# Kernel tuning notes

Hardware: AMD Instinct MI355X
Metric: run time of the kernel (lower is better)

## Reference

```python
import jax, jax.numpy as jnp
import numpy as np


def setup_inputs() -> dict:
    key = jax.random.key(0)
    k1, k2 = jax.random.split(key)
    B, C, N = 32, 512, 4096
    x = jax.random.normal(k1, (B, C, N), dtype=jnp.float32)
    gamma = jax.random.normal(k2, (1,), dtype=jnp.float32)
    return {"x": x, "gamma": gamma}


def reference(x, gamma):
    # x: [B, C, N]. Channel attention: energy = x @ x^T -> [B, C, C]
    energy = jnp.einsum('bcn,bdn->bcd', x, x)
    # inverted score: rowmax - energy, then softmax over last dim
    energy_new = jnp.max(energy, axis=-1, keepdims=True) - energy
    attention = jax.nn.softmax(energy_new, axis=-1)  # [B, C, C]
    out = jnp.einsum('bcd,bdn->bcn', attention, x)
    return gamma * out + x
```

## Files before the change

kernel.cpp:

```cpp
#include <hip/hip_runtime.h>
#include <stdint.h>
#include <stddef.h>

#define NB 32
#define NC 512
#define NN 4096
#define NSPLIT 4
#define KCH (NN / NSPLIT)

typedef _Float16 h4_t __attribute__((ext_vector_type(4)));
typedef _Float16 h8_t __attribute__((ext_vector_type(8)));
typedef float    f4_t __attribute__((ext_vector_type(4)));

__device__ __forceinline__ void gload16(const _Float16* g, _Float16* l) {
    __builtin_amdgcn_global_load_lds(
        (const __attribute__((address_space(1))) void*)g,
        (__attribute__((address_space(3))) void*)l, 16, 0, 0);
}

__global__ __launch_bounds__(256) void cast_transpose(
    const float* __restrict__ x, _Float16* __restrict__ Xh,
    _Float16* __restrict__ Xl, _Float16* __restrict__ Xt)
{
    __shared__ __attribute__((aligned(16))) _Float16 tile[64 * 66];
    const int b = blockIdx.z, c0 = blockIdx.y * 64, n0 = blockIdx.x * 64;
    const int t = threadIdx.x;
    const int lr = t >> 4;
    const int lc = (t & 15) * 4;
    const size_t xbase = (size_t)b * NC * NN;

#pragma unroll
    for (int p = 0; p < 4; ++p) {
        const int r = p * 16 + lr;
        const size_t off = xbase + (size_t)(c0 + r) * NN + (n0 + lc);
        const float4 v = *(const float4*)(x + off);
        const _Float16 h0 = (_Float16)v.x, h1 = (_Float16)v.y;
        const _Float16 h2 = (_Float16)v.z, h3 = (_Float16)v.w;
        h4_t hv = {h0, h1, h2, h3};
        *(h4_t*)(Xh + off) = hv;
        h4_t lv = {(_Float16)(v.x - (float)h0), (_Float16)(v.y - (float)h1),
                   (_Float16)(v.z - (float)h2), (_Float16)(v.w - (float)h3)};
        *(h4_t*)(Xl + off) = lv;
        tile[r * 66 + lc + 0] = h0;
        tile[r * 66 + lc + 1] = h1;
        tile[r * 66 + lc + 2] = h2;
        tile[r * 66 + lc + 3] = h3;
    }
    __syncthreads();
    const size_t tbase = (size_t)b * NN * NC;
#pragma unroll
    for (int p = 0; p < 4; ++p) {
        const int rn = p * 16 + lr;
        h4_t w;
        w[0] = tile[(lc + 0) * 66 + rn];
        w[1] = tile[(lc + 1) * 66 + rn];
        w[2] = tile[(lc + 2) * 66 + rn];
        w[3] = tile[(lc + 3) * 66 + rn];
        *(h4_t*)(Xt + tbase + (size_t)(n0 + rn) * NC + (c0 + lc)) = w;
    }
}

__global__ __launch_bounds__(256) void cast_hl(
    const float* __restrict__ x, _Float16* __restrict__ Xh,
    _Float16* __restrict__ Xl)
{
    const size_t total = (size_t)NB * NC * NN / 4;
    for (size_t i = (size_t)blockIdx.x * 256 + threadIdx.x; i < total;
         i += (size_t)gridDim.x * 256) {
        const float4 v = ((const float4*)x)[i];
        const _Float16 h0 = (_Float16)v.x, h1 = (_Float16)v.y;
        const _Float16 h2 = (_Float16)v.z, h3 = (_Float16)v.w;
        h4_t hv = {h0, h1, h2, h3};
        h4_t lv = {(_Float16)(v.x - (float)h0), (_Float16)(v.y - (float)h1),
                   (_Float16)(v.z - (float)h2), (_Float16)(v.w - (float)h3)};
        ((h4_t*)Xh)[i] = hv;
        ((h4_t*)Xl)[i] = lv;
    }
}

__global__ __launch_bounds__(256, 4) void gemm1_energy(
    const _Float16* __restrict__ Xh, const _Float16* __restrict__ Xl,
    float* __restrict__ part)
{
    __shared__ __attribute__((aligned(16))) _Float16 sAh[128 * 32];
    __shared__ __attribute__((aligned(16))) _Float16 sBh[128 * 32];
    __shared__ __attribute__((aligned(16))) _Float16 sAl[128 * 32];
    __shared__ __attribute__((aligned(16))) _Float16 sBl[128 * 32];

    const int flat = blockIdx.x;
    const int xcd  = flat & 7;
    const int slot = flat >> 3;
    const int grp  = xcd + 8 * (slot / 10);
    const int mem  = slot % 10;
    const int b    = grp >> 2;
    const int s    = grp & (NSPLIT - 1);

    const int ti = (int)((sqrtf(8.0f * (float)mem + 1.0f) - 1.0f) * 0.5f);
    const int tj = mem - ((ti * (ti + 1)) >> 1);
    const bool diag = (ti == tj);

    const int t = threadIdx.x;
    const int wave = t >> 6, lane = t & 63;
    const int srow = t >> 2, scol = (t & 3) * 8;

    const size_t xb = (size_t)b * NC * NN + (size_t)s * KCH;
    const _Float16* gAh = Xh + xb + (size_t)(ti * 128 + srow) * NN + scol;
    const _Float16* gBh = Xh + xb + (size_t)(tj * 128 + srow) * NN + scol;
    const _Float16* gAl = Xl + xb + (size_t)(ti * 128 + srow) * NN + scol;
    const _Float16* gBl = Xl + xb + (size_t)(tj * 128 + srow) * NN + scol;

    const int wr = wave >> 1, wc = wave & 1;
    const int fr = lane & 15, fko = (lane >> 4) * 8;
    const int hi4 = (lane >> 4) * 4;

    const _Float16* rBh = diag ? sAh : sBh;
    const _Float16* rBl = diag ? sAl : sBl;

    f4_t acc[4][4];
#pragma unroll
    for (int m = 0; m < 4; ++m)
#pragma unroll
        for (int n = 0; n < 4; ++n) acc[m][n] = (f4_t){0.f, 0.f, 0.f, 0.f};

    for (int k0 = 0; k0 < KCH; k0 += 32) {
        gload16(gAh + k0,                   sAh + wave * 512);
        gload16(gAh + k0 + 64 * (size_t)NN, sAh + 2048 + wave * 512);
        gload16(gAl + k0,                   sAl + wave * 512);
        gload16(gAl + k0 + 64 * (size_t)NN, sAl + 2048 + wave * 512);
        if (!diag) {
            gload16(gBh + k0,                   sBh + wave * 512);
            gload16(gBh + k0 + 64 * (size_t)NN, sBh + 2048 + wave * 512);
            gload16(gBl + k0,                   sBl + wave * 512);
            gload16(gBl + k0 + 64 * (size_t)NN, sBl + 2048 + wave * 512);
        }
        __syncthreads();

        h8_t ah[4], bh[4], al[4], bl[4];
#pragma unroll
        for (int m = 0; m < 4; ++m) {
            ah[m] = *(const h8_t*)(sAh + (wr * 64 + m * 16 + fr) * 32 + fko);
            bh[m] = *(const h8_t*)(rBh + (wc * 64 + m * 16 + fr) * 32 + fko);
            al[m] = *(const h8_t*)(sAl + (wr * 64 + m * 16 + fr) * 32 + fko);
            bl[m] = *(const h8_t*)(rBl + (wc * 64 + m * 16 + fr) * 32 + fko);
        }
#pragma unroll
        for (int m = 0; m < 4; ++m)
#pragma unroll
            for (int nf = 0; nf < 4; ++nf) {
                acc[nf][m] = __builtin_amdgcn_mfma_f32_16x16x32_f16(bh[nf], ah[m], acc[nf][m], 0, 0, 0);
                acc[nf][m] = __builtin_amdgcn_mfma_f32_16x16x32_f16(bl[nf], ah[m], acc[nf][m], 0, 0, 0);
                acc[nf][m] = __builtin_amdgcn_mfma_f32_16x16x32_f16(bh[nf], al[m], acc[nf][m], 0, 0, 0);
            }
        __syncthreads();
    }

    float* pb = part + ((size_t)s * NB + b) * (NC * NC);
#pragma unroll
    for (int m = 0; m < 4; ++m) {
        const int i = ti * 128 + wr * 64 + m * 16 + fr;
#pragma unroll
        for (int nf = 0; nf < 4; ++nf) {
            const int jjb = tj * 128 + wc * 64 + nf * 16 + hi4;
            *(f4_t*)(pb + (size_t)i * NC + jjb) = acc[nf][m];
            if (!diag) {
#pragma unroll
                for (int j = 0; j < 4; ++j)
                    pb[(size_t)(jjb + j) * NC + i] = acc[nf][m][j];
            }
        }
    }
}

__global__ __launch_bounds__(256) void softmax_inv(
    const float* __restrict__ part, _Float16* __restrict__ attn)
{
    const int row = blockIdx.x * 4 + (threadIdx.x >> 6);
    const int lane = threadIdx.x & 63;
    const size_t roff = (size_t)row * NC;

    float4 a0 = {0.f, 0.f, 0.f, 0.f}, a1 = {0.f, 0.f, 0.f, 0.f};
#pragma unroll
    for (int s = 0; s < NSPLIT; ++s) {
        const float4* p = (const float4*)(part + (size_t)s * NB * NC * NC + roff);
        const float4 v0 = p[lane], v1 = p[64 + lane];
        a0.x += v0.x; a0.y += v0.y; a0.z += v0.z; a0.w += v0.w;
        a1.x += v1.x; a1.y += v1.y; a1.z += v1.z; a1.w += v1.w;
    }

    float mn = fminf(fminf(fminf(a0.x, a0.y), fminf(a0.z, a0.w)),
                     fminf(fminf(a1.x, a1.y), fminf(a1.z, a1.w)));
#pragma unroll
    for (int off = 32; off; off >>= 1) mn = fminf(mn, __shfl_xor(mn, off));

    const float w0 = __expf(mn - a0.x), w1 = __expf(mn - a0.y);
    const float w2 = __expf(mn - a0.z), w3 = __expf(mn - a0.w);
    const float w4 = __expf(mn - a1.x), w5 = __expf(mn - a1.y);
    const float w6 = __expf(mn - a1.z), w7 = __expf(mn - a1.w);
    float sum = ((w0 + w1) + (w2 + w3)) + ((w4 + w5) + (w6 + w7));
#pragma unroll
    for (int off = 32; off; off >>= 1) sum += __shfl_xor(sum, off);
    const float inv = 1.0f / sum;

    h4_t o0 = {(_Float16)(w0 * inv), (_Float16)(w1 * inv),
               (_Float16)(w2 * inv), (_Float16)(w3 * inv)};
    h4_t o1 = {(_Float16)(w4 * inv), (_Float16)(w5 * inv),
               (_Float16)(w6 * inv), (_Float16)(w7 * inv)};
    ((h4_t*)(attn + roff))[lane] = o0;
    ((h4_t*)(attn + roff))[64 + lane] = o1;
}

__global__ __launch_bounds__(256) void transpose_h(
    const _Float16* __restrict__ Xh, _Float16* __restrict__ Xt)
{
    __shared__ __attribute__((aligned(16))) _Float16 tile[64 * 66];
    const int b = blockIdx.z, c0 = blockIdx.y * 64, n0 = blockIdx.x * 64;
    const int t = threadIdx.x;
    const int lr = t >> 4;
    const int lc = (t & 15) * 4;
    const size_t hbase = (size_t)b * NC * NN;

#pragma unroll
    for (int p = 0; p < 4; ++p) {
        const int r = p * 16 + lr;
        const h4_t v = *(const h4_t*)(Xh + hbase + (size_t)(c0 + r) * NN + (n0 + lc));
        tile[r * 66 + lc + 0] = v[0];
        tile[r * 66 + lc + 1] = v[1];
        tile[r * 66 + lc + 2] = v[2];
        tile[r * 66 + lc + 3] = v[3];
    }
    __syncthreads();
    const size_t tbase = (size_t)b * NN * NC;
#pragma unroll
    for (int p = 0; p < 4; ++p) {
        const int rn = p * 16 + lr;
        h4_t w;
        w[0] = tile[(lc + 0) * 66 + rn];
        w[1] = tile[(lc + 1) * 66 + rn];
        w[2] = tile[(lc + 2) * 66 + rn];
        w[3] = tile[(lc + 3) * 66 + rn];
        *(h4_t*)(Xt + tbase + (size_t)(n0 + rn) * NC + (c0 + lc)) = w;
    }
}

__global__ __launch_bounds__(256) void gemm2_out(
    const _Float16* __restrict__ attn, const _Float16* __restrict__ Xt,
    const _Float16* __restrict__ Xh, const float* __restrict__ gammap,
    float* __restrict__ out)
{
    __shared__ __attribute__((aligned(16))) _Float16 sA[128 * 32];
    __shared__ __attribute__((aligned(16))) _Float16 sB[128 * 32];

    const int flat = blockIdx.x;
    const int xcd  = flat & 7;
    const int slot = flat >> 3;
    const int b    = xcd + 8 * (slot >> 7);
    const int memb = slot & 127;
    const int brow = (memb & 3) * 128;
    const int bcol = (memb >> 2) * 128;

    const int t = threadIdx.x;
    const int wave = t >> 6, lane = t & 63;
    const int srow = t >> 2, scol = (t & 3) * 8;

    const _Float16* gA = attn + (size_t)b * NC * NC + (size_t)(brow + srow) * NC + scol;
    const _Float16* gB = Xt   + (size_t)b * NN * NC + (size_t)(bcol + srow) * NC + scol;

    const int wr = wave >> 1, wc = wave & 1;
    const int fr = lane & 15, fko = (lane >> 4) * 8;
    const int hi4 = (lane >> 4) * 4;

    f4_t acc[4][4];
#pragma unroll
    for (int m = 0; m < 4; ++m)
#pragma unroll
        for (int n = 0; n < 4; ++n) acc[m][n] = (f4_t){0.f, 0.f, 0.f, 0.f};

    for (int k0 = 0; k0 < NC; k0 += 32) {
        gload16(gA + k0,           sA + wave * 512);
        gload16(gA + k0 + 64 * NC, sA + 2048 + wave * 512);
        gload16(gB + k0,           sB + wave * 512);
        gload16(gB + k0 + 64 * NC, sB + 2048 + wave * 512);
        __syncthreads();

        h8_t a[4], bb[4];
#pragma unroll
        for (int m = 0; m < 4; ++m) {
            a[m]  = *(const h8_t*)(sA + (wr * 64 + m * 16 + fr) * 32 + fko);
            bb[m] = *(const h8_t*)(sB + (wc * 64 + m * 16 + fr) * 32 + fko);
        }
#pragma unroll
        for (int m = 0; m < 4; ++m)
#pragma unroll
            for (int nf = 0; nf < 4; ++nf)
                acc[nf][m] = __builtin_amdgcn_mfma_f32_16x16x32_f16(bb[nf], a[m], acc[nf][m], 0, 0, 0);
        __syncthreads();
    }

    const float g = gammap[0];
    const _Float16* xb = Xh + (size_t)b * NC * NN;
    float* ob = out + (size_t)b * NC * NN;
#pragma unroll
    for (int m = 0; m < 4; ++m) {
        const int c_ = brow + wr * 64 + m * 16 + fr;
#pragma unroll
        for (int nf = 0; nf < 4; ++nf) {
            const int n_ = bcol + wc * 64 + nf * 16 + hi4;
            const size_t off = (size_t)c_ * NN + n_;
            const h4_t xv = *(const h4_t*)(xb + off);
            f4_t o;
#pragma unroll
            for (int j = 0; j < 4; ++j)
                o[j] = g * acc[nf][m][j] + (float)xv[j];
            *(f4_t*)(ob + off) = o;
        }
    }
}

extern "C" void kernel_launch(void* const* d_in, const int* in_sizes, int n_in,
                              void* d_out, int out_size, void* d_ws, size_t ws_size,
                              hipStream_t stream)
{
    const float* x     = (const float*)d_in[0];
    const float* gamma = (const float*)d_in[1];
    float* out = (float*)d_out;
    char* ws = (char*)d_ws;

    if (ws_size >= 553648128ull) {
        _Float16* Xh   = (_Float16*)(ws);
        _Float16* Xl   = (_Float16*)(ws + 134217728ull);
        _Float16* Xt   = (_Float16*)(ws + 268435456ull);
        _Float16* attn = (_Float16*)(ws + 402653184ull);
        float*    part = (float*)   (ws + 419430400ull);

        cast_transpose<<<dim3(NN / 64, NC / 64, NB), 256, 0, stream>>>(x, Xh, Xl, Xt);
        gemm1_energy<<<dim3(10 * NSPLIT * NB), 256, 0, stream>>>(Xh, Xl, part);
        softmax_inv<<<dim3(NB * NC / 4), 256, 0, stream>>>(part, attn);
        gemm2_out<<<dim3(4096), 256, 0, stream>>>(attn, Xt, Xh, gamma, out);
    } else {
        _Float16* Xh   = (_Float16*)(ws);
        _Float16* XlXt = (_Float16*)(ws + 134217728ull);
        _Float16* attn = (_Float16*)(ws + 268435456ull);
        float*    part = (float*)   (ws + 285212672ull);

        cast_hl<<<dim3(2048), 256, 0, stream>>>(x, Xh, XlXt);
        gemm1_energy<<<dim3(10 * NSPLIT * NB), 256, 0, stream>>>(Xh, XlXt, part);
        softmax_inv<<<dim3(NB * NC / 4), 256, 0, stream>>>(part, attn);
        transpose_h<<<dim3(NN / 64, NC / 64, NB), 256, 0, stream>>>(Xh, XlXt);
        gemm2_out<<<dim3(4096), 256, 0, stream>>>(attn, XlXt, Xh, gamma, out);
    }
}
```

Baseline: 476.6 us.

## Swizzle LDS tiles and double-buffer gemm2 with A read from global

In the first GEMM, the global-to-LDS copy and the fragment reads now use an XOR swizzle on the column chunk, so the 16-byte LDS reads no longer hit the same banks. The output GEMM is restructured. The Xt tile now uses a double-buffered, swizzled LDS layout with 64-wide K steps, and the next tile is prefetched while the current one is computed. The attention (A) fragments now come straight from global memory instead of being staged through LDS. This removes LDS bank conflicts and half the barriers, and overlaps loads with MFMA work. The cost is redundant global reads of A across waves and more LDS per block.

```diff
diff --git a/kernel.cpp b/kernel.cpp
--- a/kernel.cpp
+++ b/kernel.cpp
@@ -101,7 +101,8 @@
 
     const int t = threadIdx.x;
     const int wave = t >> 6, lane = t & 63;
-    const int srow = t >> 2, scol = (t & 3) * 8;
+    const int srow = t >> 2;
+    const int scol = (((t & 3) ^ ((t >> 2) & 3)) * 8);
 
     const size_t xb = (size_t)b * NC * NN + (size_t)s * KCH;
     const _Float16* gAh = Xh + xb + (size_t)(ti * 128 + srow) * NN + scol;
@@ -112,6 +113,7 @@
     const int wr = wave >> 1, wc = wave & 1;
     const int fr = lane & 15, fko = (lane >> 4) * 8;
     const int hi4 = (lane >> 4) * 4;
+    const int fsw = fko ^ ((fr & 3) << 3);
 
     const _Float16* rBh = diag ? sAh : sBh;
     const _Float16* rBl = diag ? sAl : sBl;
@@ -138,10 +140,10 @@
         h8_t ah[4], bh[4], al[4], bl[4];
 #pragma unroll
         for (int m = 0; m < 4; ++m) {
-            ah[m] = *(const h8_t*)(sAh + (wr * 64 + m * 16 + fr) * 32 + fko);
-            bh[m] = *(const h8_t*)(rBh + (wc * 64 + m * 16 + fr) * 32 + fko);
-            al[m] = *(const h8_t*)(sAl + (wr * 64 + m * 16 + fr) * 32 + fko);
-            bl[m] = *(const h8_t*)(rBl + (wc * 64 + m * 16 + fr) * 32 + fko);
+            ah[m] = *(const h8_t*)(sAh + (wr * 64 + m * 16 + fr) * 32 + fsw);
+            bh[m] = *(const h8_t*)(rBh + (wc * 64 + m * 16 + fr) * 32 + fsw);
+            al[m] = *(const h8_t*)(sAl + (wr * 64 + m * 16 + fr) * 32 + fsw);
+            bl[m] = *(const h8_t*)(rBl + (wc * 64 + m * 16 + fr) * 32 + fsw);
         }
 #pragma unroll
         for (int m = 0; m < 4; ++m)
@@ -247,8 +249,7 @@
     const _Float16* __restrict__ Xh, const float* __restrict__ gammap,
     float* __restrict__ out)
 {
-    __shared__ __attribute__((aligned(16))) _Float16 sA[128 * 32];
-    __shared__ __attribute__((aligned(16))) _Float16 sB[128 * 32];
+    __shared__ __attribute__((aligned(16))) _Float16 sB[2][128 * 64];
 
     const int flat = blockIdx.x;
     const int xcd  = flat & 7;
@@ -260,14 +261,15 @@
 
     const int t = threadIdx.x;
     const int wave = t >> 6, lane = t & 63;
-    const int srow = t >> 2, scol = (t & 3) * 8;
-
-    const _Float16* gA = attn + (size_t)b * NC * NC + (size_t)(brow + srow) * NC + scol;
-    const _Float16* gB = Xt   + (size_t)b * NN * NC + (size_t)(bcol + srow) * NC + scol;
-
     const int wr = wave >> 1, wc = wave & 1;
     const int fr = lane & 15, fko = (lane >> 4) * 8;
     const int hi4 = (lane >> 4) * 4;
+    const int bsw = (fr & 7) << 3;
+
+    const int rr = t >> 3;
+    const int sck = (((t & 7) ^ (rr & 7)) * 8);
+    const _Float16* gB = Xt + (size_t)b * NN * NC + (size_t)bcol * NC;
+    const _Float16* gA = attn + (size_t)b * NC * NC;
 
     f4_t acc[4][4];
 #pragma unroll
@@ -275,26 +277,50 @@
 #pragma unroll
         for (int n = 0; n < 4; ++n) acc[m][n] = (f4_t){0.f, 0.f, 0.f, 0.f};
 
-    for (int k0 = 0; k0 < NC; k0 += 32) {
-        gload16(gA + k0,           sA + wave * 512);
-        gload16(gA + k0 + 64 * NC, sA + 2048 + wave * 512);
-        gload16(gB + k0,           sB + wave * 512);
-        gload16(gB + k0 + 64 * NC, sB + 2048 + wave * 512);
+#define STAGE_B(buf, k0)                                                     \
+    {                                                                        \
+        _Pragma("unroll")                                                    \
+        for (int p = 0; p < 4; ++p)                                          \
+            gload16(gB + (size_t)(p * 32 + rr) * NC + (k0) + sck,            \
+                    &sB[buf][0] + p * 2048 + wave * 512 + (lane)*8);         \
+    }
+
+    STAGE_B(0, 0);
+    __syncthreads();
+
+    int cur = 0;
+#pragma unroll
+    for (int it = 0; it < 8; ++it) {
+        const int k0 = it * 64;
+        if (it < 7) STAGE_B(cur ^ 1, k0 + 64);
+
+        h8_t a_[4][2];
+#pragma unroll
+        for (int m = 0; m < 4; ++m) {
+            const size_t ar = (size_t)(brow + wr * 64 + m * 16 + fr) * NC + k0;
+            a_[m][0] = *(const h8_t*)(gA + ar + fko);
+            a_[m][1] = *(const h8_t*)(gA + ar + 32 + fko);
+        }
+#pragma unroll
+        for (int kk = 0; kk < 2; ++kk) {
+            h8_t b_[4];
+#pragma unroll
+            for (int nf = 0; nf < 4; ++nf) {
+                const int row = wc * 64 + nf * 16 + fr;
+                b_[nf] = *(const h8_t*)(&sB[cur][0] + row * 64 +
+                                        ((kk * 32 + fko) ^ bsw));
+            }
+#pragma unroll
+            for (int m = 0; m < 4; ++m)
+#pragma unroll
+                for (int nf = 0; nf < 4; ++nf)
+                    acc[nf][m] = __builtin_amdgcn_mfma_f32_16x16x32_f16(
+                        b_[nf], a_[m][kk], acc[nf][m], 0, 0, 0);
+        }
         __syncthreads();
-
-        h8_t a[4], bb[4];
-#pragma unroll
-        for (int m = 0; m < 4; ++m) {
-            a[m]  = *(const h8_t*)(sA + (wr * 64 + m * 16 + fr) * 32 + fko);
-            bb[m] = *(const h8_t*)(sB + (wc * 64 + m * 16 + fr) * 32 + fko);
-        }
-#pragma unroll
-        for (int m = 0; m < 4; ++m)
-#pragma unroll
-            for (int nf = 0; nf < 4; ++nf)
-                acc[nf][m] = __builtin_amdgcn_mfma_f32_16x16x32_f16(bb[nf], a[m], acc[nf][m], 0, 0, 0);
-        __syncthreads();
-    }
+        cur ^= 1;
+    }
+#undef STAGE_B
 
     const float g = gammap[0];
     const _Float16* xb = Xh + (size_t)b * NC * NN;
```

Measured after the change: 523.7 us. 9.9% more time.
